# Kernel optimization log

Measured on AMD Instinct MI355X. Metric: run time of the kernel, lower is better.

Reference implementation:

```python
import jax, jax.numpy as jnp
import numpy as np

D = 768    # text_feature_dim (BERT)
H = 1024   # hidden_dim
L = 16384  # history length


def setup_inputs() -> dict:
    key = jax.random.key(0)
    ks = jax.random.split(key, 10)
    text_v = jax.random.normal(ks[0], (1, D), dtype=jnp.float32)
    result = jax.random.uniform(ks[1], (1,), dtype=jnp.float32)
    text_s = jax.random.normal(ks[2], (L, D), dtype=jnp.float32)
    hidden_s = jax.random.normal(ks[3], (L, H), dtype=jnp.float32)
    # GRU params (PyTorch layout: W_ih [3H, 2D], W_hh [3H, H]), uniform(-1/sqrt(H), 1/sqrt(H))
    s = 1.0 / np.sqrt(H)
    W_ih = jax.random.uniform(ks[4], (3 * H, 2 * D), minval=-s, maxval=s, dtype=jnp.float32)
    W_hh = jax.random.uniform(ks[5], (3 * H, H), minval=-s, maxval=s, dtype=jnp.float32)
    b_ih = jax.random.uniform(ks[6], (3 * H,), minval=-s, maxval=s, dtype=jnp.float32)
    b_hh = jax.random.uniform(ks[7], (3 * H,), minval=-s, maxval=s, dtype=jnp.float32)
    # score layer: Linear(D+H, 1)
    s2 = 1.0 / np.sqrt(D + H)
    score_W = jax.random.uniform(ks[8], (1, D + H), minval=-s2, maxval=s2, dtype=jnp.float32)
    score_b = jax.random.uniform(ks[9], (1,), minval=-s2, maxval=s2, dtype=jnp.float32)
    return {"text_v": text_v, "result": result, "text_s": text_s, "hidden_s": hidden_s,
            "W_ih": W_ih, "W_hh": W_hh, "b_ih": b_ih, "b_hh": b_hh,
            "score_W": score_W, "score_b": score_b}


def reference(text_v, result, text_s, hidden_s, W_ih, W_hh, b_ih, b_hh, score_W, score_b):
    # --- attention over growing history ---
    h = hidden_s[-1:, :]                                   # [1, H] last hidden state
    alpha = jax.nn.softmax(text_s @ text_v.T, axis=0)      # [L, 1]
    attn_h = alpha.T @ hidden_s                            # [1, H]

    # --- score prediction ---
    pred_v = jnp.concatenate([text_v, attn_h], axis=1)     # [1, D+H]
    score = pred_v @ score_W.T + score_b                   # [1, 1]

    # --- input gating by correctness ---
    zeros = jnp.zeros_like(text_v)
    x_r = jnp.where(result >= 0.5,
                    jnp.concatenate([text_v, zeros], axis=1),
                    jnp.concatenate([zeros, text_v], axis=1))  # [1, 2D]

    # --- GRU cell (PyTorch gate order: r, z, n) ---
    gi = x_r @ W_ih.T + b_ih                               # [1, 3H]
    gh = h @ W_hh.T + b_hh                                 # [1, 3H]
    i_r, i_z, i_n = jnp.split(gi, 3, axis=1)
    h_r, h_z, h_n = jnp.split(gh, 3, axis=1)
    r = jax.nn.sigmoid(i_r + h_r)
    z = jax.nn.sigmoid(i_z + h_z)
    n = jnp.tanh(i_n + r * h_n)
    h_new = (1.0 - z) * n + z * h                          # [1, H]

    return score[0], h_new                                 # score.squeeze(0) -> [1]
```

## Files before the change

### kernel.cpp

```cpp
#include <hip/hip_runtime.h>
#include <math.h>

#define LL 16384
#define Dm 768
#define Hm 1024

#define ATT_B 512
#define GI_B  48
#define GH_B  64

#define WS_GI 0
#define WS_GH 3072
#define WS_PM 6144
#define WS_PS 6656
#define WS_PV 7168
#define WS_M2 (7168 + 512*1024)
#define WS_S2 (WS_M2 + 16)
#define WS_V2 (WS_S2 + 16)

__device__ __forceinline__ float dot4(float4 a, float4 b) {
    return a.x*b.x + a.y*b.y + a.z*b.z + a.w*b.w;
}

__global__ __launch_bounds__(256) void k_main(
    const float* __restrict__ text_v, const float* __restrict__ result,
    const float* __restrict__ text_s, const float* __restrict__ hidden_s,
    const float* __restrict__ W_ih, const float* __restrict__ W_hh,
    const float* __restrict__ b_ih, const float* __restrict__ b_hh,
    float* __restrict__ ws)
{
    const int b    = blockIdx.x;
    const int tid  = threadIdx.x;
    const int lane = tid & 63;
    const int wv   = tid >> 6;

    if (b < ATT_B) {
        __shared__ float dots[32];
        __shared__ float wts[32];
        const int row0 = b * 32;
        float4 tv0 = *(const float4*)(text_v + 4*lane);
        float4 tv1 = *(const float4*)(text_v + 4*lane + 256);
        float4 tv2 = *(const float4*)(text_v + 4*lane + 512);
        #pragma unroll
        for (int i = 0; i < 8; ++i) {
            const int rl = wv*8 + i;
            const float* p = text_s + (size_t)(row0 + rl)*Dm + 4*lane;
            float4 x0 = *(const float4*)(p);
            float4 x1 = *(const float4*)(p + 256);
            float4 x2 = *(const float4*)(p + 512);
            float s = dot4(x0, tv0) + dot4(x1, tv1) + dot4(x2, tv2);
            #pragma unroll
            for (int o = 32; o; o >>= 1) s += __shfl_xor(s, o);
            if (lane == 0) dots[rl] = s;
        }
        __syncthreads();
        float m = dots[0];
        #pragma unroll
        for (int r = 1; r < 32; ++r) m = fmaxf(m, dots[r]);
        if (tid < 32) wts[tid] = expf(dots[tid] - m);
        __syncthreads();
        float4 acc = {0.f, 0.f, 0.f, 0.f};
        for (int r = 0; r < 32; ++r) {
            const float w = wts[r];
            const float4 hv = *(const float4*)(hidden_s + (size_t)(row0 + r)*Hm + 4*tid);
            acc.x += w*hv.x; acc.y += w*hv.y; acc.z += w*hv.z; acc.w += w*hv.w;
        }
        *(float4*)(ws + WS_PV + (size_t)b*1024 + 4*tid) = acc;
        if (tid == 0) {
            float s = 0.f;
            #pragma unroll
            for (int r = 0; r < 32; ++r) s += wts[r];
            ws[WS_PM + b] = m;
            ws[WS_PS + b] = s;
        }
    } else if (b < ATT_B + GI_B) {
        const int gb = b - ATT_B;
        const int off = (result[0] >= 0.5f) ? 0 : Dm;
        float4 tv0 = *(const float4*)(text_v + 4*lane);
        float4 tv1 = *(const float4*)(text_v + 4*lane + 256);
        float4 tv2 = *(const float4*)(text_v + 4*lane + 512);
        const int kbase = gb*64 + wv*16;
        #pragma unroll
        for (int i = 0; i < 16; ++i) {
            const int k = kbase + i;
            const float* p = W_ih + (size_t)k*(2*Dm) + off + 4*lane;
            float4 x0 = *(const float4*)(p);
            float4 x1 = *(const float4*)(p + 256);
            float4 x2 = *(const float4*)(p + 512);
            float s = dot4(x0, tv0) + dot4(x1, tv1) + dot4(x2, tv2);
            #pragma unroll
            for (int o = 32; o; o >>= 1) s += __shfl_xor(s, o);
            if (lane == 0) ws[WS_GI + k] = s + b_ih[k];
        }
    } else {
        const int hb = b - ATT_B - GI_B;
        const float* h = hidden_s + (size_t)(LL - 1)*Hm;
        float4 h0 = *(const float4*)(h + 4*lane);
        float4 h1 = *(const float4*)(h + 4*lane + 256);
        float4 h2 = *(const float4*)(h + 4*lane + 512);
        float4 h3 = *(const float4*)(h + 4*lane + 768);
        const int kbase = hb*48 + wv*12;
        #pragma unroll
        for (int i = 0; i < 12; ++i) {
            const int k = kbase + i;
            const float* p = W_hh + (size_t)k*Hm + 4*lane;
            float4 x0 = *(const float4*)(p);
            float4 x1 = *(const float4*)(p + 256);
            float4 x2 = *(const float4*)(p + 512);
            float4 x3 = *(const float4*)(p + 768);
            float s = dot4(x0, h0) + dot4(x1, h1) + dot4(x2, h2) + dot4(x3, h3);
            #pragma unroll
            for (int o = 32; o; o >>= 1) s += __shfl_xor(s, o);
            if (lane == 0) ws[WS_GH + k] = s + b_hh[k];
        }
    }
}

__global__ __launch_bounds__(256) void k_mid(float* __restrict__ ws) {
    __shared__ float sc[32];
    const int b = blockIdx.x;
    const int t = threadIdx.x;
    const int p0 = b * 32;
    float m = ws[WS_PM + p0];
    #pragma unroll
    for (int r = 1; r < 32; ++r) m = fmaxf(m, ws[WS_PM + p0 + r]);
    if (t < 32) sc[t] = expf(ws[WS_PM + p0 + t] - m);
    __syncthreads();
    float4 acc = {0.f, 0.f, 0.f, 0.f};
    for (int r = 0; r < 32; ++r) {
        const float w = sc[r];
        const float4 v = *(const float4*)(ws + WS_PV + (size_t)(p0 + r)*1024 + 4*t);
        acc.x += w*v.x; acc.y += w*v.y; acc.z += w*v.z; acc.w += w*v.w;
    }
    *(float4*)(ws + WS_V2 + (size_t)b*1024 + 4*t) = acc;
    if (t == 0) {
        float s = 0.f;
        #pragma unroll
        for (int r = 0; r < 32; ++r) s += sc[r] * ws[WS_PS + p0 + r];
        ws[WS_M2 + b] = m;
        ws[WS_S2 + b] = s;
    }
}

__global__ __launch_bounds__(1024) void k_final(
    const float* __restrict__ text_v, const float* __restrict__ hidden_s,
    const float* __restrict__ score_W, const float* __restrict__ score_b,
    float* __restrict__ ws, float* __restrict__ out)
{
    __shared__ float sred[16];
    const int tid = threadIdx.x;
    float M = ws[WS_M2];
    #pragma unroll
    for (int r = 1; r < 16; ++r) M = fmaxf(M, ws[WS_M2 + r]);
    float S = 0.f, a = 0.f;
    #pragma unroll
    for (int r = 0; r < 16; ++r) {
        const float scl = expf(ws[WS_M2 + r] - M);
        S += scl * ws[WS_S2 + r];
        a += scl * ws[WS_V2 + r*1024 + tid];
    }
    a /= S;
    float sp = a * score_W[Dm + tid];
    if (tid < Dm) sp += text_v[tid] * score_W[tid];
    #pragma unroll
    for (int o = 32; o; o >>= 1) sp += __shfl_xor(sp, o);
    if ((tid & 63) == 0) sred[tid >> 6] = sp;
    __syncthreads();
    if (tid == 0) {
        float s = score_b[0];
        #pragma unroll
        for (int i = 0; i < 16; ++i) s += sred[i];
        out[0] = s;
    }
    const float gi_r = ws[WS_GI + tid];
    const float gi_z = ws[WS_GI + 1024 + tid];
    const float gi_n = ws[WS_GI + 2048 + tid];
    const float gh_r = ws[WS_GH + tid];
    const float gh_z = ws[WS_GH + 1024 + tid];
    const float gh_n = ws[WS_GH + 2048 + tid];
    const float hprev = hidden_s[(size_t)(LL - 1)*Hm + tid];
    const float r = 1.f / (1.f + expf(-(gi_r + gh_r)));
    const float z = 1.f / (1.f + expf(-(gi_z + gh_z)));
    const float n = tanhf(gi_n + r*gh_n);
    out[1 + tid] = (1.f - z)*n + z*hprev;
}

extern "C" void kernel_launch(void* const* d_in, const int* in_sizes, int n_in,
                              void* d_out, int out_size, void* d_ws, size_t ws_size,
                              hipStream_t stream) {
    const float* text_v   = (const float*)d_in[0];
    const float* result   = (const float*)d_in[1];
    const float* text_s   = (const float*)d_in[2];
    const float* hidden_s = (const float*)d_in[3];
    const float* W_ih     = (const float*)d_in[4];
    const float* W_hh     = (const float*)d_in[5];
    const float* b_ih     = (const float*)d_in[6];
    const float* b_hh     = (const float*)d_in[7];
    const float* score_W  = (const float*)d_in[8];
    const float* score_b  = (const float*)d_in[9];
    float* out = (float*)d_out;
    float* ws  = (float*)d_ws;

    k_main <<<ATT_B + GI_B + GH_B, 256, 0, stream>>>(
        text_v, result, text_s, hidden_s, W_ih, W_hh, b_ih, b_hh, ws);
    k_mid  <<<16, 256,  0, stream>>>(ws);
    k_final<<<1,  1024, 0, stream>>>(text_v, hidden_s, score_W, score_b, ws, out);
}
```

Baseline: 194.5 us.

## Double grid size and batch-prefetch loads into registers across attention and GEMV blocks

The attention partition goes from 32 rows to 16 rows per block, giving 1024 attention blocks. The GI and GH GEMV blocks now handle 16 output rows each (192 blocks apiece). All three paths issue every load for a block into register arrays before computing, and the hidden_s and partial-vector accumulations prefetch in groups of 8 rows with double buffering. The intent is more parallelism and more memory requests in flight for this bandwidth-bound kernel. The cost is a larger partial workspace (1024x1024 floats written and re-read by k_mid), twice the k_mid blocks, and higher register pressure.

```diff
diff --git a/kernel.cpp b/kernel.cpp
--- a/kernel.cpp
+++ b/kernel.cpp
@@ -5,18 +5,19 @@
 #define Dm 768
 #define Hm 1024
 
-#define ATT_B 512
-#define GI_B  48
-#define GH_B  64
+#define ATT_B 1024
+#define GI_B  192
+#define GH_B  192
+#define MID_B 32
 
 #define WS_GI 0
 #define WS_GH 3072
 #define WS_PM 6144
-#define WS_PS 6656
-#define WS_PV 7168
-#define WS_M2 (7168 + 512*1024)
-#define WS_S2 (WS_M2 + 16)
-#define WS_V2 (WS_S2 + 16)
+#define WS_PS 7168
+#define WS_PV 8192
+#define WS_M2 (8192 + 1024*1024)
+#define WS_S2 (WS_M2 + 32)
+#define WS_V2 (WS_S2 + 32)
 
 __device__ __forceinline__ float dot4(float4 a, float4 b) {
     return a.x*b.x + a.y*b.y + a.z*b.z + a.w*b.w;
@@ -35,61 +36,87 @@
     const int wv   = tid >> 6;
 
     if (b < ATT_B) {
-        __shared__ float dots[32];
-        __shared__ float wts[32];
-        const int row0 = b * 32;
+        __shared__ float dots[16];
+        __shared__ float wts[16];
+        const int row0  = b * 16;
+        const int rbase = wv * 4;
+
         float4 tv0 = *(const float4*)(text_v + 4*lane);
         float4 tv1 = *(const float4*)(text_v + 4*lane + 256);
         float4 tv2 = *(const float4*)(text_v + 4*lane + 512);
-        #pragma unroll
-        for (int i = 0; i < 8; ++i) {
-            const int rl = wv*8 + i;
-            const float* p = text_s + (size_t)(row0 + rl)*Dm + 4*lane;
-            float4 x0 = *(const float4*)(p);
-            float4 x1 = *(const float4*)(p + 256);
-            float4 x2 = *(const float4*)(p + 512);
-            float s = dot4(x0, tv0) + dot4(x1, tv1) + dot4(x2, tv2);
+
+        float4 x[4][3];
+        #pragma unroll
+        for (int i = 0; i < 4; ++i) {
+            const float* p = text_s + (size_t)(row0 + rbase + i)*Dm + 4*lane;
+            x[i][0] = *(const float4*)(p);
+            x[i][1] = *(const float4*)(p + 256);
+            x[i][2] = *(const float4*)(p + 512);
+        }
+        #pragma unroll
+        for (int i = 0; i < 4; ++i) {
+            float s = dot4(x[i][0], tv0) + dot4(x[i][1], tv1) + dot4(x[i][2], tv2);
             #pragma unroll
             for (int o = 32; o; o >>= 1) s += __shfl_xor(s, o);
-            if (lane == 0) dots[rl] = s;
-        }
+            if (lane == 0) dots[rbase + i] = s;
+        }
+
+        float4 hv[2][8];
+        #pragma unroll
+        for (int r = 0; r < 8; ++r)
+            hv[0][r] = *(const float4*)(hidden_s + (size_t)(row0 + r)*Hm + 4*tid);
+
         __syncthreads();
         float m = dots[0];
         #pragma unroll
-        for (int r = 1; r < 32; ++r) m = fmaxf(m, dots[r]);
-        if (tid < 32) wts[tid] = expf(dots[tid] - m);
+        for (int r = 1; r < 16; ++r) m = fmaxf(m, dots[r]);
+        if (tid < 16) wts[tid] = expf(dots[tid] - m);
         __syncthreads();
+
         float4 acc = {0.f, 0.f, 0.f, 0.f};
-        for (int r = 0; r < 32; ++r) {
-            const float w = wts[r];
-            const float4 hv = *(const float4*)(hidden_s + (size_t)(row0 + r)*Hm + 4*tid);
-            acc.x += w*hv.x; acc.y += w*hv.y; acc.z += w*hv.z; acc.w += w*hv.w;
+        #pragma unroll
+        for (int c = 0; c < 2; ++c) {
+            if (c < 1) {
+                #pragma unroll
+                for (int r = 0; r < 8; ++r)
+                    hv[1][r] = *(const float4*)(hidden_s + (size_t)(row0 + 8 + r)*Hm + 4*tid);
+            }
+            #pragma unroll
+            for (int r = 0; r < 8; ++r) {
+                const float w = wts[c*8 + r];
+                acc.x += w*hv[c][r].x; acc.y += w*hv[c][r].y;
+                acc.z += w*hv[c][r].z; acc.w += w*hv[c][r].w;
+            }
         }
         *(float4*)(ws + WS_PV + (size_t)b*1024 + 4*tid) = acc;
         if (tid == 0) {
             float s = 0.f;
             #pragma unroll
-            for (int r = 0; r < 32; ++r) s += wts[r];
+            for (int r = 0; r < 16; ++r) s += wts[r];
             ws[WS_PM + b] = m;
             ws[WS_PS + b] = s;
         }
     } else if (b < ATT_B + GI_B) {
-        const int gb = b - ATT_B;
+        const int gb  = b - ATT_B;
         const int off = (result[0] >= 0.5f) ? 0 : Dm;
         float4 tv0 = *(const float4*)(text_v + 4*lane);
         float4 tv1 = *(const float4*)(text_v + 4*lane + 256);
         float4 tv2 = *(const float4*)(text_v + 4*lane + 512);
-        const int kbase = gb*64 + wv*16;
-        #pragma unroll
-        for (int i = 0; i < 16; ++i) {
+        const int kbase = gb*16 + wv*4;
+        float4 x[4][3];
+        #pragma unroll
+        for (int i = 0; i < 4; ++i) {
+            const float* p = W_ih + (size_t)(kbase + i)*(2*Dm) + off + 4*lane;
+            x[i][0] = *(const float4*)(p);
+            x[i][1] = *(const float4*)(p + 256);
+            x[i][2] = *(const float4*)(p + 512);
+        }
+        #pragma unroll
+        for (int i = 0; i < 4; ++i) {
+            float s = dot4(x[i][0], tv0) + dot4(x[i][1], tv1) + dot4(x[i][2], tv2);
+            #pragma unroll
+            for (int o = 32; o; o >>= 1) s += __shfl_xor(s, o);
             const int k = kbase + i;
-            const float* p = W_ih + (size_t)k*(2*Dm) + off + 4*lane;
-            float4 x0 = *(const float4*)(p);
-            float4 x1 = *(const float4*)(p + 256);
-            float4 x2 = *(const float4*)(p + 512);
-            float s = dot4(x0, tv0) + dot4(x1, tv1) + dot4(x2, tv2);
-            #pragma unroll
-            for (int o = 32; o; o >>= 1) s += __shfl_xor(s, o);
             if (lane == 0) ws[WS_GI + k] = s + b_ih[k];
         }
     } else {
@@ -99,38 +126,60 @@
         float4 h1 = *(const float4*)(h + 4*lane + 256);
         float4 h2 = *(const float4*)(h + 4*lane + 512);
         float4 h3 = *(const float4*)(h + 4*lane + 768);
-        const int kbase = hb*48 + wv*12;
-        #pragma unroll
-        for (int i = 0; i < 12; ++i) {
+        const int kbase = hb*16 + wv*4;
+        float4 x[4][4];
+        #pragma unroll
+        for (int i = 0; i < 4; ++i) {
+            const float* p = W_hh + (size_t)(kbase + i)*Hm + 4*lane;
+            x[i][0] = *(const float4*)(p);
+            x[i][1] = *(const float4*)(p + 256);
+            x[i][2] = *(const float4*)(p + 512);
+            x[i][3] = *(const float4*)(p + 768);
+        }
+        #pragma unroll
+        for (int i = 0; i < 4; ++i) {
+            float s = dot4(x[i][0], h0) + dot4(x[i][1], h1)
+                    + dot4(x[i][2], h2) + dot4(x[i][3], h3);
+            #pragma unroll
+            for (int o = 32; o; o >>= 1) s += __shfl_xor(s, o);
             const int k = kbase + i;
-            const float* p = W_hh + (size_t)k*Hm + 4*lane;
-            float4 x0 = *(const float4*)(p);
-            float4 x1 = *(const float4*)(p + 256);
-            float4 x2 = *(const float4*)(p + 512);
-            float4 x3 = *(const float4*)(p + 768);
-            float s = dot4(x0, h0) + dot4(x1, h1) + dot4(x2, h2) + dot4(x3, h3);
-            #pragma unroll
-            for (int o = 32; o; o >>= 1) s += __shfl_xor(s, o);
             if (lane == 0) ws[WS_GH + k] = s + b_hh[k];
         }
     }
 }
 
 __global__ __launch_bounds__(256) void k_mid(float* __restrict__ ws) {
+    __shared__ float sm[32];
     __shared__ float sc[32];
-    const int b = blockIdx.x;
-    const int t = threadIdx.x;
+    const int b  = blockIdx.x;
+    const int t  = threadIdx.x;
     const int p0 = b * 32;
-    float m = ws[WS_PM + p0];
-    #pragma unroll
-    for (int r = 1; r < 32; ++r) m = fmaxf(m, ws[WS_PM + p0 + r]);
-    if (t < 32) sc[t] = expf(ws[WS_PM + p0 + t] - m);
+    if (t < 32) sm[t] = ws[WS_PM + p0 + t];
     __syncthreads();
+    float m = sm[0];
+    #pragma unroll
+    for (int r = 1; r < 32; ++r) m = fmaxf(m, sm[r]);
+    if (t < 32) sc[t] = expf(sm[t] - m);
+    __syncthreads();
+
     float4 acc = {0.f, 0.f, 0.f, 0.f};
-    for (int r = 0; r < 32; ++r) {
-        const float w = sc[r];
-        const float4 v = *(const float4*)(ws + WS_PV + (size_t)(p0 + r)*1024 + 4*t);
-        acc.x += w*v.x; acc.y += w*v.y; acc.z += w*v.z; acc.w += w*v.w;
+    float4 hv[2][8];
+    #pragma unroll
+    for (int r = 0; r < 8; ++r)
+        hv[0][r] = *(const float4*)(ws + WS_PV + (size_t)(p0 + r)*1024 + 4*t);
+    #pragma unroll
+    for (int c = 0; c < 4; ++c) {
+        if (c < 3) {
+            #pragma unroll
+            for (int r = 0; r < 8; ++r)
+                hv[(c+1)&1][r] = *(const float4*)(ws + WS_PV + (size_t)(p0 + (c+1)*8 + r)*1024 + 4*t);
+        }
+        #pragma unroll
+        for (int r = 0; r < 8; ++r) {
+            const float w = sc[c*8 + r];
+            acc.x += w*hv[c&1][r].x; acc.y += w*hv[c&1][r].y;
+            acc.z += w*hv[c&1][r].z; acc.w += w*hv[c&1][r].w;
+        }
     }
     *(float4*)(ws + WS_V2 + (size_t)b*1024 + 4*t) = acc;
     if (t == 0) {
@@ -151,10 +200,10 @@
     const int tid = threadIdx.x;
     float M = ws[WS_M2];
     #pragma unroll
-    for (int r = 1; r < 16; ++r) M = fmaxf(M, ws[WS_M2 + r]);
+    for (int r = 1; r < 32; ++r) M = fmaxf(M, ws[WS_M2 + r]);
     float S = 0.f, a = 0.f;
     #pragma unroll
-    for (int r = 0; r < 16; ++r) {
+    for (int r = 0; r < 32; ++r) {
         const float scl = expf(ws[WS_M2 + r] - M);
         S += scl * ws[WS_S2 + r];
         a += scl * ws[WS_V2 + r*1024 + tid];
@@ -203,6 +252,6 @@
 
     k_main <<<ATT_B + GI_B + GH_B, 256, 0, stream>>>(
         text_v, result, text_s, hidden_s, W_ih, W_hh, b_ih, b_hh, ws);
-    k_mid  <<<16, 256,  0, stream>>>(ws);
-    k_final<<<1,  1024, 0, stream>>>(text_v, hidden_s, score_W, score_b, ws, out);
-}
+    k_mid  <<<MID_B, 256, 0, stream>>>(ws);
+    k_final<<<1, 1024, 0, stream>>>(text_v, hidden_s, score_W, score_b, ws, out);
+}
```

New measurement: 187.5 us. 1.04x faster.
